# Kernel tuning notes

Measured on AMD Instinct MI355X. Metric: run time of the kernel, lower is better.

## Reference

```python
import jax, jax.numpy as jnp
import numpy as np

# SwitchNet f* dims
B = 1024
Nb1, Nw1 = 8, 10          # input: Nb1^2=64 blocks, window 2*Nw1^2=200
Nb2x, Nb2y = 8, 8
Nw2x, Nw2y = 10, 10
R = 16
J1 = Nb1 * Nb1            # 64
K1 = 2 * Nw1 * Nw1        # 200
L1 = Nb2x * Nb2y * R      # 1024
J2 = Nb2x * Nb2y * J1     # 4096
J3 = Nb2x * Nb2y          # 64
K3 = J1 * R               # 1024
L3 = 2 * Nw2x * Nw2y      # 200


def _dm(x, kernel, bias):
    # per-block batched GEMM: x [B, J, K] @ kernel [J, K, L] + bias [1, J, L]
    return jnp.einsum('ijk,jkl->ijl', x, kernel) + bias


def setup_inputs() -> dict:
    key = jax.random.key(0)
    ks = jax.random.split(key, 7)
    u = lambda k, shape: jax.random.uniform(k, shape, dtype=jnp.float32) * 0.01
    return {
        'x': jax.random.normal(ks[0], (B, Nb1 * Nw1 * Nb1 * Nw1, 2), dtype=jnp.float32),
        'k1': u(ks[1], (J1, K1, L1)),
        'b1': u(ks[2], (1, J1, L1)),
        'k2': u(ks[3], (J2, R, R)),
        'b2': u(ks[4], (1, J2, R)),
        'k3': u(ks[5], (J3, K3, L3)),
        'b3': u(ks[6], (1, J3, L3)),
    }


def reference(x, k1, b1, k2, b2, k3, b3):
    bs = x.shape[0]
    # gather input windows: [B, Nb1, Nw1, Nb1, Nw1, 2] -> block-major
    h = x.reshape(bs, Nb1, Nw1, Nb1, Nw1, 2)
    h = h.transpose(0, 1, 3, 2, 4, 5)
    h = h.reshape(bs, J1, K1)
    h = _dm(h, k1, b1)                                   # [B, 64, 1024]
    h = h.reshape(bs, J1, Nb2x * Nb2y, R)
    h = h.transpose(0, 3, 1, 2)                          # [B, r, 64, 64]
    h = h.reshape(bs, J2, R)
    h = _dm(h, k2, b2)                                   # [B, 4096, r]
    h = h.reshape(bs, J3, K3)
    h = _dm(h, k3, b3)                                   # [B, 64, 200]
    h = h.reshape(bs, Nb2x, Nb2y, Nw2x, Nw2y, 2)
    h = h.transpose(0, 1, 3, 2, 4, 5)
    return h.reshape(bs, Nb2x * Nw2x, Nb2y * Nw2y, 2)   # [B, 80, 80, 2]
```

## Files before the change

### kernel.cpp

```cpp
#include <hip/hip_runtime.h>

typedef __attribute__((ext_vector_type(8))) short short8;
typedef __attribute__((ext_vector_type(4))) short bfx4;
typedef __attribute__((ext_vector_type(4))) float floatx4;

__device__ __forceinline__ float bf2f(short u) {
  unsigned int i = ((unsigned int)(unsigned short)u) << 16;
  return __builtin_bit_cast(float, i);
}
__device__ __forceinline__ short f2bf(float f) {
  unsigned int x = __builtin_bit_cast(unsigned int, f);
  x += 0x7fffu + ((x >> 16) & 1u);
  return (short)(x >> 16);
}

__device__ __forceinline__ void gl_lds16(const short* g, short* lds) {
  __builtin_amdgcn_global_load_lds(
      (const __attribute__((address_space(1))) unsigned int*)g,
      (__attribute__((address_space(3))) unsigned int*)lds, 16, 0, 0);
}

#define BC 256

__global__ __launch_bounds__(256) void gather_x(const float* __restrict__ x,
                                                short* __restrict__ hA, int bOffset) {
  int tid = blockIdx.x * 256 + threadIdx.x;
  const int total = 64 * BC * 224;
  if (tid >= total) return;
  int kp = tid % 224;
  int rem = tid / 224;
  int b_loc = rem & (BC - 1);
  int j1 = rem / BC;
  short v = 0;
  if (kp < 200) {
    int c = kp & 1;
    int w = kp >> 1;
    int wx = w / 10;
    int wy = w - wx * 10;
    int bx = j1 >> 3, by = j1 & 7;
    v = f2bf(x[(size_t)(bOffset + b_loc) * 12800 +
               ((size_t)(bx * 800 + wx * 80 + by * 10 + wy)) * 2 + c]);
  }
  hA[tid] = v;
}

__global__ __launch_bounds__(256) void transpose_k1(const float* __restrict__ k1,
                                                    short* __restrict__ k1t) {
  const int j1 = blockIdx.x;
  const int nBase = blockIdx.y * 64;
  const int kBase = blockIdx.z * 56;
  __shared__ short tr[64][68];
  const int t = threadIdx.x;
  const int nl = t & 63;
  const int ksub = t >> 6;
  const float* src = k1 + (size_t)j1 * 204800 + (size_t)kBase * 1024 + nBase + nl;
#pragma unroll
  for (int pass = 0; pass < 14; ++pass) {
    int kloc = pass * 4 + ksub;
    int k = kBase + kloc;
    tr[nl][kloc] = (k < 200) ? f2bf(src[kloc * 1024]) : (short)0;
  }
  __syncthreads();
  short* dstbase = k1t + ((size_t)j1 * 1024 + nBase) * 224 + kBase;
#pragma unroll
  for (int p = 0; p < 4; ++p) {
    int u = p * 256 + t;
    int row = u >> 4;
    int kq = u & 15;
    if (kq < 14) {
      bfx4 v = *(const bfx4*)&tr[row][kq * 4];
      *(bfx4*)&dstbase[row * 224 + kq * 4] = v;
    }
  }
}

__global__ __launch_bounds__(256) void transpose_k3(const float* __restrict__ k3,
                                                    short* __restrict__ k3t) {
  const int j3 = blockIdx.x;
  const int kBase = blockIdx.y * 128;
  const int nBase = blockIdx.z * 64;
  __shared__ short tr[64][132];
  const int t = threadIdx.x;
  const int nl = t & 63;
  const int ksub = t >> 6;
  const int nGlob = nBase + nl;
  const bool valid = (nGlob < 200);
  const float* src = k3 + (size_t)j3 * 204800 + (size_t)kBase * 200 + nGlob;
#pragma unroll 4
  for (int pass = 0; pass < 32; ++pass) {
    int k = pass * 4 + ksub;
    tr[nl][k] = valid ? f2bf(src[k * 200]) : (short)0;
  }
  __syncthreads();
  short* dstbase = k3t + ((size_t)j3 * 256 + nBase) * 1024 + kBase;
#pragma unroll
  for (int pass = 0; pass < 8; ++pass) {
    int idx = (pass * 256 + t) * 4;
    int row = idx >> 7;
    int koff = idx & 127;
    bfx4 v = *(const bfx4*)&tr[row][koff];
    *(bfx4*)&dstbase[row * 1024 + koff] = v;
  }
}

__global__ __launch_bounds__(256) void gemm_stage1(const short* __restrict__ hA,
                                                   const short* __restrict__ k1t,
                                                   const float* __restrict__ b1,
                                                   short* __restrict__ h1) {
  const int j1 = blockIdx.z;
  const int mBase = blockIdx.y * 128;
  const int nBase = blockIdx.x * 128;
  __shared__ short As[128 * 32];
  __shared__ short Bs[128 * 32];
  const int tid = threadIdx.x;
  const int lane = tid & 63;
  const int wave = tid >> 6;
  const int quad = lane >> 4;
  const int l16 = lane & 15;
  const int wm = wave >> 1, wn = wave & 1;
  const int ldRow = tid >> 2;
  const int ldCol = (tid & 3) * 8;
  const short* Aj = hA + (size_t)j1 * BC * 224 + (size_t)(mBase + ldRow) * 224 + ldCol;
  const short* Bj = k1t + (size_t)j1 * 1024 * 224 + (size_t)(nBase + ldRow) * 224 + ldCol;
  short* ldsA = &As[tid * 8];
  short* ldsB = &Bs[tid * 8];
  floatx4 acc[4][4] = {};

  for (int kk = 0; kk < 224; kk += 32) {
    __syncthreads();
    gl_lds16(Aj + kk, ldsA);
    gl_lds16(Aj + 64 * 224 + kk, ldsA + 64 * 32);
    gl_lds16(Bj + kk, ldsB);
    gl_lds16(Bj + 64 * 224 + kk, ldsB + 64 * 32);
    __syncthreads();
    short8 af[4], bf[4];
#pragma unroll
    for (int mt = 0; mt < 4; ++mt)
      af[mt] = *(const short8*)&As[(wm * 64 + mt * 16 + l16) * 32 + quad * 8];
#pragma unroll
    for (int nt = 0; nt < 4; ++nt)
      bf[nt] = *(const short8*)&Bs[(wn * 64 + nt * 16 + l16) * 32 + quad * 8];
#pragma unroll
    for (int mt = 0; mt < 4; ++mt)
#pragma unroll
      for (int nt = 0; nt < 4; ++nt)
        acc[mt][nt] =
            __builtin_amdgcn_mfma_f32_16x16x32_bf16(af[mt], bf[nt], acc[mt][nt], 0, 0, 0);
  }
#pragma unroll
  for (int nt = 0; nt < 4; ++nt) {
    int n = nBase + wn * 64 + nt * 16 + l16;
    float bias = b1[j1 * 1024 + n];
#pragma unroll
    for (int mt = 0; mt < 4; ++mt) {
#pragma unroll
      for (int r = 0; r < 4; ++r) {
        int m = mBase + wm * 64 + mt * 16 + quad * 4 + r;
        h1[((size_t)j1 * BC + m) * 1024 + n] = f2bf(acc[mt][nt][r] + bias);
      }
    }
  }
}

__global__ __launch_bounds__(256) void stage2(const short* __restrict__ h1,
                                              const float* __restrict__ k2,
                                              const float* __restrict__ b2,
                                              short* __restrict__ h2p, int mTot,
                                              int bOff2) {
  const int j1 = blockIdx.x;
  const int bBase = blockIdx.y * 8;
  __shared__ short in_s[8][1024];
  __shared__ short w_s[256 * 66];
  __shared__ float bias_s[16 * 64];
  const int tid = threadIdx.x;
#pragma unroll
  for (int ii = 0; ii < 4; ++ii) {
    int flat = (ii * 256 + tid) * 8;
    int b_loc = flat >> 10;
    int k = flat & 1023;
    *(short8*)&in_s[b_loc][k] =
        *(const short8*)&h1[((size_t)j1 * BC + bBase + b_loc) * 1024 + k];
  }
#pragma unroll
  for (int ii = 0; ii < 16; ++ii) {
    int flat = (ii * 256 + tid) * 4;
    int blk = flat >> 8;
    int within = flat & 255;
    int r = blk >> 2, b2hi = blk & 3;
    int j2 = r * 256 + j1 * 4 + b2hi;
    floatx4 v = *(const floatx4*)&k2[(size_t)j2 * 256 + within];
#pragma unroll
    for (int i = 0; i < 4; ++i) w_s[(within + i) * 66 + blk] = f2bf(v[i]);
  }
  {
    int blk = tid >> 2;
    int r2o = (tid & 3) * 4;
    int r = blk >> 2, b2hi = blk & 3;
    int j2 = r * 256 + j1 * 4 + b2hi;
#pragma unroll
    for (int i = 0; i < 4; ++i) bias_s[(r2o + i) * 64 + blk] = b2[j2 * 16 + r2o + i];
  }
  __syncthreads();
#pragma unroll
  for (int i4 = 0; i4 < 2; ++i4) {
    int idx = i4 * 256 + tid;
    int b_loc = idx >> 6;
    int rem = idx & 63;
    int r = rem >> 2;
    int b2hi = rem & 3;
    float acc[16];
#pragma unroll
    for (int r2 = 0; r2 < 16; ++r2) acc[r2] = bias_s[r2 * 64 + rem];
#pragma unroll
    for (int k = 0; k < 16; ++k) {
      float iv = bf2f(in_s[b_loc][(b2hi * 16 + k) * 16 + r]);
#pragma unroll
      for (int r2 = 0; r2 < 16; ++r2)
        acc[r2] += iv * bf2f(w_s[(k * 16 + r2) * 66 + rem]);
    }
    int j3 = r * 4 + (j1 >> 4);
    int k3o = (j1 & 15) * 64 + b2hi * 16;
    short8 o0, o1;
#pragma unroll
    for (int t = 0; t < 8; ++t) {
      o0[t] = f2bf(acc[t]);
      o1[t] = f2bf(acc[8 + t]);
    }
    short* dst = h2p + ((size_t)j3 * mTot + bOff2 + bBase + b_loc) * 1024 + k3o;
    *(short8*)&dst[0] = o0;
    *(short8*)&dst[8] = o1;
  }
}

__global__ __launch_bounds__(256) void gemm_stage3(const short* __restrict__ h2p,
                                                   const short* __restrict__ k3t,
                                                   const float* __restrict__ b3,
                                                   float* __restrict__ out, int mTot,
                                                   int bOffset) {
  const int j3 = blockIdx.z;
  const int mBase = blockIdx.y * 128;
  const int nBase = blockIdx.x * 128;
  __shared__ short As[128 * 32];
  __shared__ short Bs[128 * 32];
  const int tid = threadIdx.x;
  const int lane = tid & 63;
  const int wave = tid >> 6;
  const int quad = lane >> 4;
  const int l16 = lane & 15;
  const int wm = wave >> 1, wn = wave & 1;
  const int ldRow = tid >> 2;
  const int ldCol = (tid & 3) * 8;
  const short* Aj =
      h2p + (size_t)j3 * mTot * 1024 + (size_t)(mBase + ldRow) * 1024 + ldCol;
  const short* Bj =
      k3t + (size_t)j3 * 256 * 1024 + (size_t)(nBase + ldRow) * 1024 + ldCol;
  short* ldsA = &As[tid * 8];
  short* ldsB = &Bs[tid * 8];
  floatx4 acc[4][4] = {};

  for (int kk = 0; kk < 1024; kk += 32) {
    __syncthreads();
    gl_lds16(Aj + kk, ldsA);
    gl_lds16(Aj + 64 * 1024 + kk, ldsA + 64 * 32);
    gl_lds16(Bj + kk, ldsB);
    gl_lds16(Bj + 64 * 1024 + kk, ldsB + 64 * 32);
    __syncthreads();
    short8 af[4], bf[4];
#pragma unroll
    for (int mt = 0; mt < 4; ++mt)
      af[mt] = *(const short8*)&As[(wm * 64 + mt * 16 + l16) * 32 + quad * 8];
#pragma unroll
    for (int nt = 0; nt < 4; ++nt)
      bf[nt] = *(const short8*)&Bs[(wn * 64 + nt * 16 + l16) * 32 + quad * 8];
#pragma unroll
    for (int mt = 0; mt < 4; ++mt)
#pragma unroll
      for (int nt = 0; nt < 4; ++nt)
        acc[mt][nt] =
            __builtin_amdgcn_mfma_f32_16x16x32_bf16(af[mt], bf[nt], acc[mt][nt], 0, 0, 0);
  }
  const int B2x = j3 >> 3, B2y = j3 & 7;
#pragma unroll
  for (int nt = 0; nt < 4; ++nt) {
    int n = nBase + wn * 64 + nt * 16 + l16;
    if (n < 200) {
      float bias = b3[j3 * 200 + n];
      int c = n & 1;
      int t = n >> 1;
      int w2x = t / 10, w2y = t - w2x * 10;
      int orow = B2x * 10 + w2x, ocol = B2y * 10 + w2y;
#pragma unroll
      for (int mt = 0; mt < 4; ++mt) {
#pragma unroll
        for (int r = 0; r < 4; ++r) {
          int m = bOffset + mBase + wm * 64 + mt * 16 + quad * 4 + r;
          out[(((size_t)m * 80 + orow) * 80 + ocol) * 2 + c] = acc[mt][nt][r] + bias;
        }
      }
    }
  }
}

extern "C" void kernel_launch(void* const* d_in, const int* in_sizes, int n_in,
                              void* d_out, int out_size, void* d_ws, size_t ws_size,
                              hipStream_t stream) {
  const float* x = (const float*)d_in[0];
  const float* k1 = (const float*)d_in[1];
  const float* b1 = (const float*)d_in[2];
  const float* k2 = (const float*)d_in[3];
  const float* b2 = (const float*)d_in[4];
  const float* k3 = (const float*)d_in[5];
  const float* b3 = (const float*)d_in[6];
  float* out = (float*)d_out;
  char* ws = (char*)d_ws;

  short* k1t = (short*)(ws);
  short* k3t = (short*)(ws + 29360128);
  short* hA = (short*)(ws + 62914560);
  short* h1c = (short*)(ws + 70254592);
  short* h2p = (short*)(ws + 103809024);

  const bool full = (ws_size >= 238026752ull);
  const int mTot = full ? 1024 : BC;

  transpose_k1<<<dim3(64, 16, 4), 256, 0, stream>>>(k1, k1t);
  transpose_k3<<<dim3(64, 8, 4), 256, 0, stream>>>(k3, k3t);
  for (int c = 0; c < 1024 / BC; ++c) {
    int bOffset = c * BC;
    gather_x<<<(64 * BC * 224) / 256, 256, 0, stream>>>(x, hA, bOffset);
    gemm_stage1<<<dim3(8, BC / 128, 64), 256, 0, stream>>>(hA, k1t, b1, h1c);
    stage2<<<dim3(64, BC / 8), 256, 0, stream>>>(h1c, k2, b2, h2p, mTot,
                                                 full ? bOffset : 0);
    if (!full)
      gemm_stage3<<<dim3(2, BC / 128, 64), 256, 0, stream>>>(h2p, k3t, b3, out, BC,
                                                             bOffset);
  }
  if (full)
    gemm_stage3<<<dim3(2, 1024 / 128, 64), 256, 0, stream>>>(h2p, k3t, b3, out, 1024,
                                                             0);
}
```

Before: 582.3 us.

## Double-buffer LDS tiles and remap block IDs across XCDs in stage GEMMs

Both the stage-1 and stage-3 GEMM kernels now keep two LDS buffers per operand. Each iteration prefetches the next K-slice with global_load_lds while the current slice feeds the MFMAs, so only one barrier per iteration is needed instead of two. The kernels also compute a flattened, permuted block index so that consecutive blocks sharing operands land on the same XCD, which is meant to improve L2 reuse. The cost is double the LDS footprint, possibly lower occupancy, and a remap that assumes particular grid shapes (power-of-two gridDim.y, block counts divisible by 8). The compiler may also insert conservative vmcnt waits that limit the intended overlap.

```diff
diff --git a/kernel.cpp b/kernel.cpp
--- a/kernel.cpp
+++ b/kernel.cpp
@@ -107,11 +107,13 @@
                                                    const short* __restrict__ k1t,
                                                    const float* __restrict__ b1,
                                                    short* __restrict__ h1) {
-  const int j1 = blockIdx.z;
-  const int mBase = blockIdx.y * 128;
-  const int nBase = blockIdx.x * 128;
-  __shared__ short As[128 * 32];
-  __shared__ short Bs[128 * 32];
+  int bid = (int)blockIdx.x + 8 * (int)blockIdx.y + 16 * (int)blockIdx.z;
+  bid = ((bid & 7) << 7) | (bid >> 3);
+  const int nBase = (bid & 7) * 128;
+  const int mBase = ((bid >> 3) & 1) * 128;
+  const int j1 = bid >> 4;
+  __shared__ short As[2][128 * 32];
+  __shared__ short Bs[2][128 * 32];
   const int tid = threadIdx.x;
   const int lane = tid & 63;
   const int wave = tid >> 6;
@@ -122,30 +124,37 @@
   const int ldCol = (tid & 3) * 8;
   const short* Aj = hA + (size_t)j1 * BC * 224 + (size_t)(mBase + ldRow) * 224 + ldCol;
   const short* Bj = k1t + (size_t)j1 * 1024 * 224 + (size_t)(nBase + ldRow) * 224 + ldCol;
-  short* ldsA = &As[tid * 8];
-  short* ldsB = &Bs[tid * 8];
+  const int lo = tid * 8;
   floatx4 acc[4][4] = {};
 
+  gl_lds16(Aj, &As[0][lo]);
+  gl_lds16(Aj + 64 * 224, &As[0][lo + 2048]);
+  gl_lds16(Bj, &Bs[0][lo]);
+  gl_lds16(Bj + 64 * 224, &Bs[0][lo + 2048]);
+  int buf = 0;
   for (int kk = 0; kk < 224; kk += 32) {
     __syncthreads();
-    gl_lds16(Aj + kk, ldsA);
-    gl_lds16(Aj + 64 * 224 + kk, ldsA + 64 * 32);
-    gl_lds16(Bj + kk, ldsB);
-    gl_lds16(Bj + 64 * 224 + kk, ldsB + 64 * 32);
-    __syncthreads();
-    short8 af[4], bf[4];
+    if (kk + 32 < 224) {
+      const int nb = buf ^ 1;
+      gl_lds16(Aj + kk + 32, &As[nb][lo]);
+      gl_lds16(Aj + 64 * 224 + kk + 32, &As[nb][lo + 2048]);
+      gl_lds16(Bj + kk + 32, &Bs[nb][lo]);
+      gl_lds16(Bj + 64 * 224 + kk + 32, &Bs[nb][lo + 2048]);
+    }
+    short8 af[4], bfv[4];
 #pragma unroll
     for (int mt = 0; mt < 4; ++mt)
-      af[mt] = *(const short8*)&As[(wm * 64 + mt * 16 + l16) * 32 + quad * 8];
+      af[mt] = *(const short8*)&As[buf][(wm * 64 + mt * 16 + l16) * 32 + quad * 8];
 #pragma unroll
     for (int nt = 0; nt < 4; ++nt)
-      bf[nt] = *(const short8*)&Bs[(wn * 64 + nt * 16 + l16) * 32 + quad * 8];
+      bfv[nt] = *(const short8*)&Bs[buf][(wn * 64 + nt * 16 + l16) * 32 + quad * 8];
 #pragma unroll
     for (int mt = 0; mt < 4; ++mt)
 #pragma unroll
       for (int nt = 0; nt < 4; ++nt)
         acc[mt][nt] =
-            __builtin_amdgcn_mfma_f32_16x16x32_bf16(af[mt], bf[nt], acc[mt][nt], 0, 0, 0);
+            __builtin_amdgcn_mfma_f32_16x16x32_bf16(af[mt], bfv[nt], acc[mt][nt], 0, 0, 0);
+    buf ^= 1;
   }
 #pragma unroll
   for (int nt = 0; nt < 4; ++nt) {
@@ -237,11 +246,16 @@
                                                    const float* __restrict__ b3,
                                                    float* __restrict__ out, int mTot,
                                                    int bOffset) {
-  const int j3 = blockIdx.z;
-  const int mBase = blockIdx.y * 128;
-  const int nBase = blockIdx.x * 128;
-  __shared__ short As[128 * 32];
-  __shared__ short Bs[128 * 32];
+  const int gy = (int)gridDim.y;
+  int bid = (int)blockIdx.x + 2 * ((int)blockIdx.y + gy * (int)blockIdx.z);
+  const int cpx = (gy << 4);
+  bid = (bid & 7) * cpx + (bid >> 3);
+  const int nBase = (bid & 1) * 128;
+  const int rest = bid >> 1;
+  const int mBase = (rest & (gy - 1)) * 128;
+  const int j3 = rest / gy;
+  __shared__ short As[2][128 * 32];
+  __shared__ short Bs[2][128 * 32];
   const int tid = threadIdx.x;
   const int lane = tid & 63;
   const int wave = tid >> 6;
@@ -254,30 +268,37 @@
       h2p + (size_t)j3 * mTot * 1024 + (size_t)(mBase + ldRow) * 1024 + ldCol;
   const short* Bj =
       k3t + (size_t)j3 * 256 * 1024 + (size_t)(nBase + ldRow) * 1024 + ldCol;
-  short* ldsA = &As[tid * 8];
-  short* ldsB = &Bs[tid * 8];
+  const int lo = tid * 8;
   floatx4 acc[4][4] = {};
 
+  gl_lds16(Aj, &As[0][lo]);
+  gl_lds16(Aj + 64 * 1024, &As[0][lo + 2048]);
+  gl_lds16(Bj, &Bs[0][lo]);
+  gl_lds16(Bj + 64 * 1024, &Bs[0][lo + 2048]);
+  int buf = 0;
   for (int kk = 0; kk < 1024; kk += 32) {
     __syncthreads();
-    gl_lds16(Aj + kk, ldsA);
-    gl_lds16(Aj + 64 * 1024 + kk, ldsA + 64 * 32);
-    gl_lds16(Bj + kk, ldsB);
-    gl_lds16(Bj + 64 * 1024 + kk, ldsB + 64 * 32);
-    __syncthreads();
-    short8 af[4], bf[4];
+    if (kk + 32 < 1024) {
+      const int nb = buf ^ 1;
+      gl_lds16(Aj + kk + 32, &As[nb][lo]);
+      gl_lds16(Aj + 64 * 1024 + kk + 32, &As[nb][lo + 2048]);
+      gl_lds16(Bj + kk + 32, &Bs[nb][lo]);
+      gl_lds16(Bj + 64 * 1024 + kk + 32, &Bs[nb][lo + 2048]);
+    }
+    short8 af[4], bfv[4];
 #pragma unroll
     for (int mt = 0; mt < 4; ++mt)
-      af[mt] = *(const short8*)&As[(wm * 64 + mt * 16 + l16) * 32 + quad * 8];
+      af[mt] = *(const short8*)&As[buf][(wm * 64 + mt * 16 + l16) * 32 + quad * 8];
 #pragma unroll
     for (int nt = 0; nt < 4; ++nt)
-      bf[nt] = *(const short8*)&Bs[(wn * 64 + nt * 16 + l16) * 32 + quad * 8];
+      bfv[nt] = *(const short8*)&Bs[buf][(wn * 64 + nt * 16 + l16) * 32 + quad * 8];
 #pragma unroll
     for (int mt = 0; mt < 4; ++mt)
 #pragma unroll
       for (int nt = 0; nt < 4; ++nt)
         acc[mt][nt] =
-            __builtin_amdgcn_mfma_f32_16x16x32_bf16(af[mt], bf[nt], acc[mt][nt], 0, 0, 0);
+            __builtin_amdgcn_mfma_f32_16x16x32_bf16(af[mt], bfv[nt], acc[mt][nt], 0, 0, 0);
+    buf ^= 1;
   }
   const int B2x = j3 >> 3, B2y = j3 & 7;
 #pragma unroll
```

Result: slower. 594.2 us (+2.0%).

## Deepen stage-3 K tile to 64 with XOR-swizzled LDS and block remap

Applied to the files above, without the earlier changes.

The stage-3 GEMM now loads 64-wide K slices per iteration instead of 32, which halves the number of barrier pairs per K loop. The LDS tiles use an XOR swizzle on 16-byte chunks to avoid bank conflicts on the fragment reads. Block IDs are remapped so that consecutive blocks are spread across what is likely the chip's XCDs (8 per group), to improve L2 locality. In exchange, LDS use doubles, and the remap assumes gy is a power of two and that the grid divides evenly.

```diff
diff --git a/kernel.cpp b/kernel.cpp
--- a/kernel.cpp
+++ b/kernel.cpp
@@ -237,47 +237,60 @@
                                                    const float* __restrict__ b3,
                                                    float* __restrict__ out, int mTot,
                                                    int bOffset) {
-  const int j3 = blockIdx.z;
-  const int mBase = blockIdx.y * 128;
-  const int nBase = blockIdx.x * 128;
-  __shared__ short As[128 * 32];
-  __shared__ short Bs[128 * 32];
+  const int gy = (int)gridDim.y;
+  int bid = (int)blockIdx.x + 2 * ((int)blockIdx.y + gy * (int)blockIdx.z);
+  const int cpx = (gy << 4);
+  bid = (bid & 7) * cpx + (bid >> 3);
+  const int nBase = (bid & 1) * 128;
+  const int rest = bid >> 1;
+  const int mBase = (rest & (gy - 1)) * 128;
+  const int j3 = rest / gy;
+  __shared__ short As[128 * 64];
+  __shared__ short Bs[128 * 64];
   const int tid = threadIdx.x;
   const int lane = tid & 63;
   const int wave = tid >> 6;
   const int quad = lane >> 4;
   const int l16 = lane & 15;
   const int wm = wave >> 1, wn = wave & 1;
-  const int ldRow = tid >> 2;
-  const int ldCol = (tid & 3) * 8;
+  const int sRow = tid >> 3;
+  const int sCol = ((tid & 7) ^ (sRow & 7)) * 8;
   const short* Aj =
-      h2p + (size_t)j3 * mTot * 1024 + (size_t)(mBase + ldRow) * 1024 + ldCol;
+      h2p + (size_t)j3 * mTot * 1024 + (size_t)(mBase + sRow) * 1024 + sCol;
   const short* Bj =
-      k3t + (size_t)j3 * 256 * 1024 + (size_t)(nBase + ldRow) * 1024 + ldCol;
+      k3t + (size_t)j3 * 256 * 1024 + (size_t)(nBase + sRow) * 1024 + sCol;
   short* ldsA = &As[tid * 8];
   short* ldsB = &Bs[tid * 8];
   floatx4 acc[4][4] = {};
 
-  for (int kk = 0; kk < 1024; kk += 32) {
+  for (int kk = 0; kk < 1024; kk += 64) {
     __syncthreads();
-    gl_lds16(Aj + kk, ldsA);
-    gl_lds16(Aj + 64 * 1024 + kk, ldsA + 64 * 32);
-    gl_lds16(Bj + kk, ldsB);
-    gl_lds16(Bj + 64 * 1024 + kk, ldsB + 64 * 32);
+#pragma unroll
+    for (int c = 0; c < 4; ++c) {
+      gl_lds16(Aj + c * 32 * 1024 + kk, ldsA + c * 2048);
+      gl_lds16(Bj + c * 32 * 1024 + kk, ldsB + c * 2048);
+    }
     __syncthreads();
-    short8 af[4], bf[4];
-#pragma unroll
-    for (int mt = 0; mt < 4; ++mt)
-      af[mt] = *(const short8*)&As[(wm * 64 + mt * 16 + l16) * 32 + quad * 8];
-#pragma unroll
-    for (int nt = 0; nt < 4; ++nt)
-      bf[nt] = *(const short8*)&Bs[(wn * 64 + nt * 16 + l16) * 32 + quad * 8];
-#pragma unroll
-    for (int mt = 0; mt < 4; ++mt)
-#pragma unroll
-      for (int nt = 0; nt < 4; ++nt)
-        acc[mt][nt] =
-            __builtin_amdgcn_mfma_f32_16x16x32_bf16(af[mt], bf[nt], acc[mt][nt], 0, 0, 0);
+#pragma unroll
+    for (int ks = 0; ks < 2; ++ks) {
+      short8 af[4], bfv[4];
+#pragma unroll
+      for (int mt = 0; mt < 4; ++mt) {
+        int r = wm * 64 + mt * 16 + l16;
+        af[mt] = *(const short8*)&As[r * 64 + ((ks * 4 + quad) ^ (l16 & 7)) * 8];
+      }
+#pragma unroll
+      for (int nt = 0; nt < 4; ++nt) {
+        int r = wn * 64 + nt * 16 + l16;
+        bfv[nt] = *(const short8*)&Bs[r * 64 + ((ks * 4 + quad) ^ (l16 & 7)) * 8];
+      }
+#pragma unroll
+      for (int mt = 0; mt < 4; ++mt)
+#pragma unroll
+        for (int nt = 0; nt < 4; ++nt)
+          acc[mt][nt] = __builtin_amdgcn_mfma_f32_16x16x32_bf16(af[mt], bfv[nt],
+                                                                acc[mt][nt], 0, 0, 0);
+    }
   }
   const int B2x = j3 >> 3, B2y = j3 & 7;
 #pragma unroll
```

New measurement: 568.9 us. 2.3% less time.
